# Kernel tuning notes

Measured on AMD Instinct MI355X. Metric: run time of the kernel, lower is better.

## Reference

```python
import jax, jax.numpy as jnp
import numpy as np

N_NODES = 100000
N_EDGES = 1200000
D_IN, D_HID, D_OUT = 64, 64, 34


def setup_inputs() -> dict:
    key = jax.random.key(0)
    k1, k2, k3, k4 = jax.random.split(key, 4)
    x = jax.random.normal(k1, (N_NODES, D_IN), dtype=jnp.float32)
    edge_index = jax.random.randint(k2, (2, N_EDGES), 0, N_NODES, dtype=jnp.int32)
    W1 = jax.random.normal(k3, (D_IN, D_HID), dtype=jnp.float32) * (1.0 / np.sqrt(D_IN))
    b1 = jnp.zeros((D_HID,), dtype=jnp.float32)
    W2 = jax.random.normal(k4, (D_HID, D_OUT), dtype=jnp.float32) * (1.0 / np.sqrt(D_HID))
    b2 = jnp.zeros((D_OUT,), dtype=jnp.float32)
    return {"x": x, "edge_index": edge_index, "W1": W1, "b1": b1, "W2": W2, "b2": b2}


def _gcn_conv(x, W, b, src, dst, norm, n_nodes):
    """PyG GCNConv: out[i] = sum_{(j->i)} norm_e * (x @ W)[j] + b."""
    xw = x @ W                                    # [N, d_out]
    msg = xw[src] * norm[:, None]                 # per-edge gather + scale
    return jax.ops.segment_sum(msg, dst, num_segments=n_nodes) + b


def reference(x, edge_index, W1, b1, W2, b2):
    n = x.shape[0]
    # add self-loops (GCNConv default add_self_loops=True)
    loops = jnp.arange(n, dtype=edge_index.dtype)
    src = jnp.concatenate([edge_index[0], loops])
    dst = jnp.concatenate([edge_index[1], loops])
    # symmetric normalization: deg^{-1/2}[src] * deg^{-1/2}[dst], deg from dst
    deg = jax.ops.segment_sum(jnp.ones_like(src, dtype=x.dtype), dst, num_segments=n)
    dinv = jnp.where(deg > 0, jax.lax.rsqrt(jnp.maximum(deg, 1e-12)), 0.0)
    norm = dinv[src] * dinv[dst]

    h = _gcn_conv(x, W1, b1, src, dst, norm, n)
    h = jax.nn.relu(h)
    h = jax.nn.softmax(h, axis=1)  # nn.Softmax() on 2D input -> dim=1
    out = _gcn_conv(h, W2, b2, src, dst, norm, n)
    return out
```

## Files before the change

### kernel.cpp

```cpp
#include <hip/hip_runtime.h>
#include <hip/hip_fp16.h>

#define D     64
#define DOUT  34
#define CAP   44
#define BSH   7
#define BW    (1 << BSH)
#define EPB   4096
#define CCAP  26
#define NPW   2
#define TB    3
#define GN1   16
#define GN2   8
#define HST   72

typedef _Float16 f16x8 __attribute__((ext_vector_type(8)));
typedef float    f32x4 __attribute__((ext_vector_type(4)));

__global__ void k_part(const int* __restrict__ ei, int E, int nblk, int nbins,
                       int* __restrict__ binned, int* __restrict__ cnt2d) {
    __shared__ int2 ebuf[EPB];
    __shared__ int  lcnt[1024];
    int b    = blockIdx.x;
    int base = b * EPB;
    int nE   = E - base; if (nE > EPB) nE = EPB;
    for (int i = threadIdx.x; i < nE; i += 256)
        ebuf[i] = make_int2(ei[base + i], ei[E + base + i]);
    for (int i = threadIdx.x; i < nbins; i += 256) lcnt[i] = 0;
    __syncthreads();
    for (int i = threadIdx.x; i < nE; i += 256) {
        int2 e  = ebuf[i];
        int bin = e.y >> BSH;
        int pos = atomicAdd(&lcnt[bin], 1);
        if (pos < CCAP)
            binned[((size_t)bin * nblk + b) * CCAP + pos] = (e.x << BSH) | (e.y & (BW - 1));
    }
    __syncthreads();
    for (int i = threadIdx.x; i < nbins; i += 256) {
        int c = lcnt[i]; if (c > CCAP) c = CCAP;
        cnt2d[(size_t)i * nblk + b] = c;
    }
}

__global__ void k_build(const int* __restrict__ binned, const int* __restrict__ cnt2d,
                        int nblk, int* __restrict__ cnt, float* __restrict__ dinv,
                        int* __restrict__ bucket, int N) {
    __shared__ int lc2d[512];
    __shared__ int lcnt[BW];
    __shared__ __align__(16) int lbuck[BW * CAP];
    int bin = blockIdx.x;
    int d0  = bin << BSH;
    for (int i = threadIdx.x; i < nblk; i += 256) lc2d[i] = cnt2d[(size_t)bin * nblk + i];
    for (int i = threadIdx.x; i < BW; i += 256) lcnt[i] = 0;
    __syncthreads();
    int totalSlots = nblk * CCAP;
    const int* bp = binned + (size_t)bin * nblk * CCAP;
    for (int i = threadIdx.x; i < totalSlots; i += 256) {
        int blk  = i / CCAP;
        int slot = i - blk * CCAP;
        if (slot < lc2d[blk]) {
            int p   = bp[i];
            int ld  = p & (BW - 1);
            int pos = atomicAdd(&lcnt[ld], 1);
            if (pos < CAP) lbuck[ld * CAP + pos] = (p >> BSH) << 6;
        }
    }
    __syncthreads();
    int nd = N - d0; if (nd > BW) nd = BW;
    for (int i = threadIdx.x; i < nd; i += 256) {
        int c = lcnt[i];
        cnt[d0 + i]  = c;
        dinv[d0 + i] = rsqrtf((float)(c + 1));
    }
    int nv = (nd * CAP) >> 2;
    int4* gb = (int4*)(bucket + (size_t)d0 * CAP);
    const int4* lb = (const int4*)lbuck;
    for (int i = threadIdx.x; i < nv; i += 256) gb[i] = lb[i];
}

__global__ void k_wconv(const float* __restrict__ W1, const float* __restrict__ W2,
                        __half* __restrict__ W1T, __half* __restrict__ W2T) {
    for (int i = threadIdx.x; i < 4096; i += 256) {
        int n = i >> 6, k = i & 63;
        W1T[i] = __float2half(W1[k * D + n]);
        W2T[i] = (n < DOUT) ? __float2half(W2[k * DOUT + n]) : __half(0.f);
    }
}

__global__ void k_gemm1m(const float* __restrict__ x, const __half* __restrict__ W1T,
                         const float* __restrict__ dinv, __half* __restrict__ xb1, int N) {
    int lane = threadIdx.x & 63;
    int wv   = threadIdx.x >> 6;
    int m    = lane & 15;
    int q    = lane >> 4;
    int rt   = blockIdx.x * 64 + wv * 16;
    int ar = rt + m; if (ar >= N) ar = N - 1;
    const float* xr = x + (size_t)ar * D + q * 8;
    float4 t0 = *(const float4*)(xr);
    float4 t1 = *(const float4*)(xr + 4);
    float4 t2 = *(const float4*)(xr + 32);
    float4 t3 = *(const float4*)(xr + 36);
    f16x8 a0, a1;
    a0[0]=(_Float16)t0.x; a0[1]=(_Float16)t0.y; a0[2]=(_Float16)t0.z; a0[3]=(_Float16)t0.w;
    a0[4]=(_Float16)t1.x; a0[5]=(_Float16)t1.y; a0[6]=(_Float16)t1.z; a0[7]=(_Float16)t1.w;
    a1[0]=(_Float16)t2.x; a1[1]=(_Float16)t2.y; a1[2]=(_Float16)t2.z; a1[3]=(_Float16)t2.w;
    a1[4]=(_Float16)t3.x; a1[5]=(_Float16)t3.y; a1[6]=(_Float16)t3.z; a1[7]=(_Float16)t3.w;
    float dr[4];
#pragma unroll
    for (int i = 0; i < 4; ++i) {
        int rr = rt + q * 4 + i;
        dr[i] = dinv[rr < N ? rr : N - 1];
    }
    const _Float16* WT = (const _Float16*)W1T;
#pragma unroll
    for (int ct = 0; ct < 4; ++ct) {
        f16x8 b0 = *(const f16x8*)(WT + (ct * 16 + m) * D + q * 8);
        f16x8 b1 = *(const f16x8*)(WT + (ct * 16 + m) * D + 32 + q * 8);
        f32x4 acc = {0.f, 0.f, 0.f, 0.f};
        acc = __builtin_amdgcn_mfma_f32_16x16x32_f16(a0, b0, acc, 0, 0, 0);
        acc = __builtin_amdgcn_mfma_f32_16x16x32_f16(a1, b1, acc, 0, 0, 0);
#pragma unroll
        for (int i = 0; i < 4; ++i) {
            int rr = rt + q * 4 + i;
            if (rr < N) xb1[(size_t)rr * D + ct * 16 + m] = __float2half(acc[i] * dr[i]);
        }
    }
}

__device__ __forceinline__ void fma8(float* a, float4 raw, float c) {
    __half2* hp = (__half2*)&raw;
#pragma unroll
    for (int k = 0; k < 4; ++k) {
        float2 f = __half22float2(hp[k]);
        a[2 * k]     = fmaf(f.x, c, a[2 * k]);
        a[2 * k + 1] = fmaf(f.y, c, a[2 * k + 1]);
    }
}

__global__ void __launch_bounds__(512, 8)
k_gather1(const int* __restrict__ cnt, const int* __restrict__ bucket,
          const __half* __restrict__ xb1, const float* __restrict__ dinv,
          const float* __restrict__ b1, const __half* __restrict__ W2T,
          __half* __restrict__ xb2, int N) {
    __shared__ int lcnt[GN1];
    __shared__ int meta[GN1 * CAP];
    __shared__ __align__(16) _Float16 hls[GN1 * HST];
    int tid  = threadIdx.x;
    int base = blockIdx.x * GN1;
    if (tid < GN1) lcnt[tid] = cnt[base + tid];
    {
        const int4* gb = (const int4*)(bucket + (size_t)base * CAP);
        int4* mb = (int4*)meta;
        for (int i = tid; i < GN1 * CAP / 4; i += 512) mb[i] = gb[i];
    }
    __syncthreads();
    int lane = tid & 63, w = tid >> 6;
    int g = lane >> 3, gl = lane & 7;
    int l0 = w * NPW;
    float4 buf[NPW][TB];
    float4 sr[NPW];
    int    nn[NPW];
#pragma unroll
    for (int j = 0; j < NPW; ++j) {
        int n = lcnt[l0 + j]; if (n > CAP) n = CAP;
        nn[j] = n;
        sr[j] = *((const float4*)(xb1 + (size_t)(base + l0 + j) * D) + gl);
#pragma unroll
        for (int t = 0; t < TB; ++t) {
            if (8 * t < n) {
                int idx = g + 8 * t;
                int mv = meta[(l0 + j) * CAP + idx];
                mv = (idx < n) ? mv : 0;
                buf[j][t] = *((const float4*)(xb1 + mv) + gl);
            }
        }
    }
    float acc[NPW][8];
#pragma unroll
    for (int j = 0; j < NPW; ++j) {
#pragma unroll
        for (int k = 0; k < 8; ++k) acc[j][k] = 0.f;
#pragma unroll
        for (int t = 0; t < TB; ++t) {
            if (8 * t < nn[j]) {
                float wv = (g + 8 * t < nn[j]) ? 1.f : 0.f;
                fma8(acc[j], buf[j][t], wv);
            }
        }
        for (int t = TB; 8 * t < nn[j]; ++t) {
            int idx = g + 8 * t;
            int mv = meta[(l0 + j) * CAP + idx];
            mv = (idx < nn[j]) ? mv : 0;
            float4 bx = *((const float4*)(xb1 + mv) + gl);
            fma8(acc[j], bx, (idx < nn[j]) ? 1.f : 0.f);
        }
    }
    const float4* b1v = (const float4*)b1;
    float4 bb0 = b1v[2 * gl], bb1 = b1v[2 * gl + 1];
    float bArr[8] = {bb0.x, bb0.y, bb0.z, bb0.w, bb1.x, bb1.y, bb1.z, bb1.w};
#pragma unroll
    for (int j = 0; j < NPW; ++j) {
#pragma unroll
        for (int k = 0; k < 8; ++k) {
            acc[j][k] += __shfl_xor(acc[j][k], 8);
            acc[j][k] += __shfl_xor(acc[j][k], 16);
            acc[j][k] += __shfl_xor(acc[j][k], 32);
        }
        fma8(acc[j], sr[j], 1.f);
        float di = dinv[base + l0 + j];
        float m = 0.f;
#pragma unroll
        for (int k = 0; k < 8; ++k) {
            acc[j][k] = fmaxf(fmaf(acc[j][k], di, bArr[k]), 0.f);
            m = fmaxf(m, acc[j][k]);
        }
#pragma unroll
        for (int o = 4; o >= 1; o >>= 1) m = fmaxf(m, __shfl_xor(m, o));
        float s = 0.f;
#pragma unroll
        for (int k = 0; k < 8; ++k) { acc[j][k] = __expf(acc[j][k] - m); s += acc[j][k]; }
#pragma unroll
        for (int o = 4; o >= 1; o >>= 1) s += __shfl_xor(s, o);
        float inv = 1.f / s;
        if (g == 0) {
            float4 st;
            __half2* sp = (__half2*)&st;
            sp[0] = __floats2half2_rn(acc[j][0] * inv, acc[j][1] * inv);
            sp[1] = __floats2half2_rn(acc[j][2] * inv, acc[j][3] * inv);
            sp[2] = __floats2half2_rn(acc[j][4] * inv, acc[j][5] * inv);
            sp[3] = __floats2half2_rn(acc[j][6] * inv, acc[j][7] * inv);
            *((float4*)(hls + (l0 + j) * HST) + gl) = st;
        }
    }
    __syncthreads();
    if (w < 4) {
        int m16 = lane & 15, q = lane >> 4;
        f16x8 a0 = *(const f16x8*)(hls + m16 * HST + q * 8);
        f16x8 a1 = *(const f16x8*)(hls + m16 * HST + 32 + q * 8);
        const _Float16* WT = (const _Float16*)W2T;
        f16x8 wb0 = *(const f16x8*)(WT + (w * 16 + m16) * D + q * 8);
        f16x8 wb1 = *(const f16x8*)(WT + (w * 16 + m16) * D + 32 + q * 8);
        f32x4 cacc = {0.f, 0.f, 0.f, 0.f};
        cacc = __builtin_amdgcn_mfma_f32_16x16x32_f16(a0, wb0, cacc, 0, 0, 0);
        cacc = __builtin_amdgcn_mfma_f32_16x16x32_f16(a1, wb1, cacc, 0, 0, 0);
#pragma unroll
        for (int i = 0; i < 4; ++i) {
            int r = base + q * 4 + i;
            xb2[(size_t)r * D + w * 16 + m16] = __float2half(cacc[i] * dinv[r]);
        }
    }
}

__global__ void __launch_bounds__(256, 8)
k_gather2(const int* __restrict__ cnt, const int* __restrict__ bucket,
          const __half* __restrict__ xb2, const float* __restrict__ dinv,
          const float* __restrict__ b2, float* __restrict__ out, int N) {
    __shared__ int lcnt[GN2];
    __shared__ int meta[GN2 * CAP];
    int tid  = threadIdx.x;
    int base = blockIdx.x * GN2;
    if (tid < GN2) lcnt[tid] = cnt[base + tid];
    {
        const int4* gb = (const int4*)(bucket + (size_t)base * CAP);
        int4* mb = (int4*)meta;
        for (int i = tid; i < GN2 * CAP / 4; i += 256) mb[i] = gb[i];
    }
    __syncthreads();
    int lane = tid & 63, w = tid >> 6;
    int g = lane >> 3, gl = lane & 7;
    int l0 = w * NPW;
    float4 buf[NPW][TB];
    float4 sr[NPW];
    int    nn[NPW];
#pragma unroll
    for (int j = 0; j < NPW; ++j) {
        int n = lcnt[l0 + j]; if (n > CAP) n = CAP;
        nn[j] = n;
        sr[j] = *((const float4*)(xb2 + (size_t)(base + l0 + j) * D) + gl);
#pragma unroll
        for (int t = 0; t < TB; ++t) {
            if (8 * t < n) {
                int idx = g + 8 * t;
                int mv = meta[(l0 + j) * CAP + idx];
                mv = (idx < n) ? mv : 0;
                buf[j][t] = *((const float4*)(xb2 + mv) + gl);
            }
        }
    }
    float acc[NPW][8];
#pragma unroll
    for (int j = 0; j < NPW; ++j) {
#pragma unroll
        for (int k = 0; k < 8; ++k) acc[j][k] = 0.f;
#pragma unroll
        for (int t = 0; t < TB; ++t) {
            if (8 * t < nn[j]) {
                float wv = (g + 8 * t < nn[j]) ? 1.f : 0.f;
                fma8(acc[j], buf[j][t], wv);
            }
        }
        for (int t = TB; 8 * t < nn[j]; ++t) {
            int idx = g + 8 * t;
            int mv = meta[(l0 + j) * CAP + idx];
            mv = (idx < nn[j]) ? mv : 0;
            float4 bx = *((const float4*)(xb2 + mv) + gl);
            fma8(acc[j], bx, (idx < nn[j]) ? 1.f : 0.f);
        }
    }
#pragma unroll
    for (int j = 0; j < NPW; ++j) {
#pragma unroll
        for (int k = 0; k < 8; ++k) {
            acc[j][k] += __shfl_xor(acc[j][k], 8);
            acc[j][k] += __shfl_xor(acc[j][k], 16);
            acc[j][k] += __shfl_xor(acc[j][k], 32);
        }
        fma8(acc[j], sr[j], 1.f);
        int r = base + l0 + j;
        float di = dinv[r];
        if (g == 0) {
            int f = 8 * gl;
#pragma unroll
            for (int k = 0; k < 8; ++k)
                if (f + k < DOUT) out[(size_t)r * DOUT + f + k] = fmaf(acc[j][k], di, b2[f + k]);
        }
    }
}

extern "C" void kernel_launch(void* const* d_in, const int* in_sizes, int n_in,
                              void* d_out, int out_size, void* d_ws, size_t ws_size,
                              hipStream_t stream) {
    const float* x  = (const float*)d_in[0];
    const int*   ei = (const int*)d_in[1];
    const float* W1 = (const float*)d_in[2];
    const float* b1 = (const float*)d_in[3];
    const float* W2 = (const float*)d_in[4];
    const float* b2 = (const float*)d_in[5];
    float* out = (float*)d_out;

    const int N = in_sizes[0] / D;
    const int E = in_sizes[1] / 2;
    const int nbins = (N + BW - 1) >> BSH;
    const int nblk  = (E + EPB - 1) / EPB;

    char*   ws     = (char*)d_ws;
    int*    cnt    = (int*)ws;
    float*  dinv   = (float*)(ws + (size_t)N * 4);
    int*    bucket = (int*)(ws + (size_t)N * 8);
    char*   U      = ws + (size_t)N * 8 + (size_t)N * CAP * 4;
    int*    binned = (int*)U;
    int*    cnt2d  = (int*)(U + (size_t)nbins * nblk * CCAP * 4);
    __half* xb1    = (__half*)U;
    __half* xb2    = xb1 + (size_t)N * D;
    __half* W1T    = (__half*)(U + (size_t)2 * N * D * 2);
    __half* W2T    = W1T + 4096;

    k_part   <<<nblk, 256, 0, stream>>>(ei, E, nblk, nbins, binned, cnt2d);
    k_build  <<<nbins, 256, 0, stream>>>(binned, cnt2d, nblk, cnt, dinv, bucket, N);
    k_wconv  <<<1, 256, 0, stream>>>(W1, W2, W1T, W2T);
    k_gemm1m <<<(N + 63) / 64, 256, 0, stream>>>(x, W1T, dinv, xb1, N);
    k_gather1<<<N / GN1, 512, 0, stream>>>(cnt, bucket, xb1, dinv, b1, W2T, xb2, N);
    k_gather2<<<N / GN2, 256, 0, stream>>>(cnt, bucket, xb2, dinv, b2, out, N);
}
```

Baseline: 224.1 us.

## Shrink layer-2 feature rows to 40 halves and trim staged neighbor metadata

Stores the layer-2 transformed features with a 40-column stride instead of 64, since only 34 outputs are needed. This cuts the bytes moved by the second gather, and only 5 of 8 lanes load data. The bucket now stores plain node indices instead of pre-shifted offsets. Only the first 24 neighbor slots per node are staged in shared memory, and the overflow tail is read directly from global memory. This reduces shared-memory footprint and staging traffic, at the cost of uncoalesced global index reads for high-degree nodes.

New measurement: 226.1 us. Within noise of the previous version (+0.9%).

```diff
diff --git a/kernel.cpp b/kernel.cpp
--- a/kernel.cpp
+++ b/kernel.cpp
@@ -10,9 +10,11 @@
 #define CCAP  26
 #define NPW   2
 #define TB    3
+#define MSLOT 24
 #define GN1   16
 #define GN2   8
 #define HST   72
+#define P2    40
 
 typedef _Float16 f16x8 __attribute__((ext_vector_type(8)));
 typedef float    f32x4 __attribute__((ext_vector_type(4)));
@@ -62,7 +64,7 @@
             int p   = bp[i];
             int ld  = p & (BW - 1);
             int pos = atomicAdd(&lcnt[ld], 1);
-            if (pos < CAP) lbuck[ld * CAP + pos] = (p >> BSH) << 6;
+            if (pos < CAP) lbuck[ld * CAP + pos] = p >> BSH;
         }
     }
     __syncthreads();
@@ -143,15 +145,18 @@
           const float* __restrict__ b1, const __half* __restrict__ W2T,
           __half* __restrict__ xb2, int N) {
     __shared__ int lcnt[GN1];
-    __shared__ int meta[GN1 * CAP];
+    __shared__ int meta[GN1 * MSLOT];
     __shared__ __align__(16) _Float16 hls[GN1 * HST];
     int tid  = threadIdx.x;
     int base = blockIdx.x * GN1;
     if (tid < GN1) lcnt[tid] = cnt[base + tid];
     {
-        const int4* gb = (const int4*)(bucket + (size_t)base * CAP);
         int4* mb = (int4*)meta;
-        for (int i = tid; i < GN1 * CAP / 4; i += 512) mb[i] = gb[i];
+        for (int i = tid; i < GN1 * (MSLOT / 4); i += 512) {
+            int node = i / (MSLOT / 4);
+            int v    = i - node * (MSLOT / 4);
+            mb[i] = ((const int4*)(bucket + (size_t)(base + node) * CAP))[v];
+        }
     }
     __syncthreads();
     int lane = tid & 63, w = tid >> 6;
@@ -169,9 +174,9 @@
         for (int t = 0; t < TB; ++t) {
             if (8 * t < n) {
                 int idx = g + 8 * t;
-                int mv = meta[(l0 + j) * CAP + idx];
+                int mv = meta[(l0 + j) * MSLOT + idx];
                 mv = (idx < n) ? mv : 0;
-                buf[j][t] = *((const float4*)(xb1 + mv) + gl);
+                buf[j][t] = *((const float4*)(xb1 + ((size_t)mv << 6)) + gl);
             }
         }
     }
@@ -189,9 +194,8 @@
         }
         for (int t = TB; 8 * t < nn[j]; ++t) {
             int idx = g + 8 * t;
-            int mv = meta[(l0 + j) * CAP + idx];
-            mv = (idx < nn[j]) ? mv : 0;
-            float4 bx = *((const float4*)(xb1 + mv) + gl);
+            int mv = (idx < nn[j]) ? bucket[(size_t)(base + l0 + j) * CAP + idx] : 0;
+            float4 bx = *((const float4*)(xb1 + ((size_t)mv << 6)) + gl);
             fma8(acc[j], bx, (idx < nn[j]) ? 1.f : 0.f);
         }
     }
@@ -233,7 +237,7 @@
         }
     }
     __syncthreads();
-    if (w < 4) {
+    if (w < 3) {
         int m16 = lane & 15, q = lane >> 4;
         f16x8 a0 = *(const f16x8*)(hls + m16 * HST + q * 8);
         f16x8 a1 = *(const f16x8*)(hls + m16 * HST + 32 + q * 8);
@@ -243,10 +247,13 @@
         f32x4 cacc = {0.f, 0.f, 0.f, 0.f};
         cacc = __builtin_amdgcn_mfma_f32_16x16x32_f16(a0, wb0, cacc, 0, 0, 0);
         cacc = __builtin_amdgcn_mfma_f32_16x16x32_f16(a1, wb1, cacc, 0, 0, 0);
-#pragma unroll
-        for (int i = 0; i < 4; ++i) {
-            int r = base + q * 4 + i;
-            xb2[(size_t)r * D + w * 16 + m16] = __float2half(cacc[i] * dinv[r]);
+        int col = w * 16 + m16;
+        if (col < P2) {
+#pragma unroll
+            for (int i = 0; i < 4; ++i) {
+                int r = base + q * 4 + i;
+                xb2[(size_t)r * P2 + col] = __float2half(cacc[i] * dinv[r]);
+            }
         }
     }
 }
@@ -256,14 +263,17 @@
           const __half* __restrict__ xb2, const float* __restrict__ dinv,
           const float* __restrict__ b2, float* __restrict__ out, int N) {
     __shared__ int lcnt[GN2];
-    __shared__ int meta[GN2 * CAP];
+    __shared__ int meta[GN2 * MSLOT];
     int tid  = threadIdx.x;
     int base = blockIdx.x * GN2;
     if (tid < GN2) lcnt[tid] = cnt[base + tid];
     {
-        const int4* gb = (const int4*)(bucket + (size_t)base * CAP);
         int4* mb = (int4*)meta;
-        for (int i = tid; i < GN2 * CAP / 4; i += 256) mb[i] = gb[i];
+        for (int i = tid; i < GN2 * (MSLOT / 4); i += 256) {
+            int node = i / (MSLOT / 4);
+            int v    = i - node * (MSLOT / 4);
+            mb[i] = ((const int4*)(bucket + (size_t)(base + node) * CAP))[v];
+        }
     }
     __syncthreads();
     int lane = tid & 63, w = tid >> 6;
@@ -276,14 +286,18 @@
     for (int j = 0; j < NPW; ++j) {
         int n = lcnt[l0 + j]; if (n > CAP) n = CAP;
         nn[j] = n;
-        sr[j] = *((const float4*)(xb2 + (size_t)(base + l0 + j) * D) + gl);
+        sr[j] = make_float4(0.f, 0.f, 0.f, 0.f);
+        if (gl < 5)
+            sr[j] = *(const float4*)(xb2 + (size_t)(base + l0 + j) * P2 + gl * 8);
 #pragma unroll
         for (int t = 0; t < TB; ++t) {
             if (8 * t < n) {
                 int idx = g + 8 * t;
-                int mv = meta[(l0 + j) * CAP + idx];
+                int mv = meta[(l0 + j) * MSLOT + idx];
                 mv = (idx < n) ? mv : 0;
-                buf[j][t] = *((const float4*)(xb2 + mv) + gl);
+                buf[j][t] = make_float4(0.f, 0.f, 0.f, 0.f);
+                if (gl < 5)
+                    buf[j][t] = *(const float4*)(xb2 + (size_t)mv * P2 + gl * 8);
             }
         }
     }
@@ -301,9 +315,10 @@
         }
         for (int t = TB; 8 * t < nn[j]; ++t) {
             int idx = g + 8 * t;
-            int mv = meta[(l0 + j) * CAP + idx];
-            mv = (idx < nn[j]) ? mv : 0;
-            float4 bx = *((const float4*)(xb2 + mv) + gl);
+            int mv = (idx < nn[j]) ? bucket[(size_t)(base + l0 + j) * CAP + idx] : 0;
+            float4 bx = make_float4(0.f, 0.f, 0.f, 0.f);
+            if (gl < 5)
+                bx = *(const float4*)(xb2 + (size_t)mv * P2 + gl * 8);
             fma8(acc[j], bx, (idx < nn[j]) ? 1.f : 0.f);
         }
     }
```
